# Kernel optimization log

Hardware: AMD Instinct MI355X
Metric: run time of the kernel (lower is better)

The kernel has to match this reference:

```python
import jax, jax.numpy as jnp
import numpy as np

H = 2048
I = 8192
E = 8
EI = I // E  # expert_intermediate_size = 1024


def setup_inputs() -> dict:
    key = jax.random.key(0)
    k1, k2, k3 = jax.random.split(key, 3)
    B, N = 4, 4096
    x = jax.random.normal(k1, (B, N, H), dtype=jnp.float32)
    position_ids = jnp.arange(B * N, dtype=jnp.int64).reshape(B, N)
    gate_up_proj = 0.02 * jax.random.normal(k2, (E, H, EI * 2), dtype=jnp.float32)
    down_proj = 0.02 * jax.random.normal(k3, (E, EI, H), dtype=jnp.float32)
    return {"x": x, "position_ids": position_ids,
            "gate_up_proj": gate_up_proj, "down_proj": down_proj}


def reference(x, position_ids, gate_up_proj, down_proj):
    # x: [B,N,H]; position_ids: [B,N] (or [N]); expert = pos % E.
    B, N, Hdim = x.shape
    if position_ids.ndim == 1:
        position_ids = jnp.broadcast_to(position_ids[None, :], (B, N))
    eids = (position_ids % E).reshape(B * N)
    flat = x.reshape(B * N, Hdim)

    # Modulo routing is perfectly balanced (N % E == 0 with sequential ids),
    # so group tokens by expert (stable sort) and run dense per-expert GEMMs
    # instead of per-token gathered-weight bmm (same math, no weight blowup).
    T = B * N
    order = jnp.argsort(eids)          # stable in jax -> tokens grouped by expert
    xg = flat[order].reshape(E, T // E, Hdim)            # [E, T/E, H]
    gu = jnp.einsum('ebh,ehk->ebk', xg, gate_up_proj)    # [E, T/E, 2*EI]
    gate, up = gu[..., :EI], gu[..., EI:]
    inter = jax.nn.silu(gate) * up                       # [E, T/E, EI]
    outg = jnp.einsum('ebi,eih->ebh', inter, down_proj)  # [E, T/E, H]
    out = jnp.zeros((T, Hdim), dtype=x.dtype).at[order].set(outg.reshape(T, Hdim))
    return out.reshape(B, N, Hdim)
```

## Files before the change

### kernel.cpp

```cpp
#include <hip/hip_runtime.h>
#include <hip/hip_bf16.h>

typedef unsigned short u16;
typedef __attribute__((ext_vector_type(8))) short short8;
typedef __attribute__((ext_vector_type(8))) unsigned short u16x8;
typedef __attribute__((ext_vector_type(4))) float f32x4;

#define H_DIM 2048
#define EI_DIM 1024
#define NEXP 8

template <int V> struct IC { static constexpr int value = V; };

__device__ __forceinline__ u16 f2bf(float f) {
  __hip_bfloat16 h = __float2bfloat16(f);
  return __builtin_bit_cast(unsigned short, h);
}

__device__ __forceinline__ void load_lds16(const void* g, void* lds) {
  __builtin_amdgcn_global_load_lds(
      (const __attribute__((address_space(1))) unsigned int*)g,
      (__attribute__((address_space(3))) unsigned int*)lds, 16, 0, 0);
}

__global__ void hist_kernel(const int* __restrict__ pid, int* __restrict__ hist) {
  int seg = blockIdx.x, lane = threadIdx.x;
  int eid = pid[seg * 64 + lane] & 7;
#pragma unroll
  for (int e = 0; e < NEXP; ++e) {
    unsigned long long m = __ballot(eid == e);
    if (lane == 0) hist[e * 256 + seg] = __popcll(m);
  }
}

__global__ void scan_kernel(const int* __restrict__ hist, int* __restrict__ base,
                            int* __restrict__ offcnt, int T) {
  __shared__ int lds[256];
  int tid = threadIdx.x;
  int v[8], s = 0;
#pragma unroll
  for (int j = 0; j < 8; ++j) { v[j] = hist[tid * 8 + j]; s += v[j]; }
  lds[tid] = s;
  __syncthreads();
  for (int d = 1; d < 256; d <<= 1) {
    int t = (tid >= d) ? lds[tid - d] : 0;
    __syncthreads();
    lds[tid] += t;
    __syncthreads();
  }
  int run = lds[tid] - s;
#pragma unroll
  for (int j = 0; j < 8; ++j) { base[tid * 8 + j] = run; run += v[j]; }
  __syncthreads();
  if (tid < NEXP) {
    int o = base[tid * 256];
    int nx = (tid < NEXP - 1) ? base[(tid + 1) * 256] : T;
    offcnt[tid] = o;
    offcnt[8 + tid] = nx - o;
  }
}

__global__ void rank_kernel(const int* __restrict__ pid, const int* __restrict__ base,
                            int* __restrict__ order) {
  int seg = blockIdx.x, lane = threadIdx.x;
  int t = seg * 64 + lane;
  int eid = pid[t] & 7;
  unsigned long long below = (1ull << lane) - 1ull;
#pragma unroll
  for (int e = 0; e < NEXP; ++e) {
    unsigned long long m = __ballot(eid == e);
    if (eid == e) {
      int r = __popcll(m & below);
      order[base[e * 256 + seg] + r] = t;
    }
  }
}

__global__ __launch_bounds__(256) void transpose_bf16(const float* __restrict__ in,
                                                      u16* __restrict__ out, int R, int C) {
  __shared__ u16 tile[64][65];
  int nbr = R >> 6, nbc = C >> 6;
  int per_e = nbr * nbc;
  int bx = blockIdx.x;
  int e = bx / per_e, rem = bx % per_e;
  int tr = rem % nbr, tc = rem / nbr;
  const float* ine = in + (size_t)e * R * C;
  u16* oute = out + (size_t)e * R * C;
  int r0 = tr * 64, c0 = tc * 64;
  int tid = threadIdx.x;
  int lrow = tid >> 4, lc4 = (tid & 15) * 4;
#pragma unroll
  for (int p = 0; p < 4; ++p) {
    int rl = p * 16 + lrow;
    float4 v = *(const float4*)&ine[(size_t)(r0 + rl) * C + c0 + lc4];
    tile[rl][lc4 + 0] = f2bf(v.x);
    tile[rl][lc4 + 1] = f2bf(v.y);
    tile[rl][lc4 + 2] = f2bf(v.z);
    tile[rl][lc4 + 3] = f2bf(v.w);
  }
  __syncthreads();
#pragma unroll
  for (int q = 0; q < 16; ++q) {
    int idx = q * 256 + tid;
    int jr = idx >> 6, hc = idx & 63;
    oute[(size_t)(c0 + jr) * R + r0 + hc] = tile[hc][jr];
  }
}

__global__ __launch_bounds__(256) void gather_x(const float* __restrict__ x,
                                                const int* __restrict__ order,
                                                u16* __restrict__ xg) {
  int g = blockIdx.x;
  int t = order[g];
  const float* src = x + (size_t)t * H_DIM;
  u16* dst = xg + (size_t)g * H_DIM;
  int c = threadIdx.x * 8;
  float4 a = *(const float4*)&src[c];
  float4 b = *(const float4*)&src[c + 4];
  u16x8 v;
  v[0] = f2bf(a.x); v[1] = f2bf(a.y); v[2] = f2bf(a.z); v[3] = f2bf(a.w);
  v[4] = f2bf(b.x); v[5] = f2bf(b.y); v[6] = f2bf(b.z); v[7] = f2bf(b.w);
  *(u16x8*)&dst[c] = v;
}

template <int KTOT, int KIND>
__device__ __forceinline__ void gemm8_body(
    const u16* __restrict__ A, const u16* __restrict__ Bmat, void* __restrict__ outp,
    const int* __restrict__ offcnt, const int* __restrict__ order, int T) {
  constexpr int NK = KTOT / 64;
  constexpr int ASTR = (KIND == 0) ? H_DIM : EI_DIM;
  constexpr int BSTR = ASTR;
  constexpr size_t BEXP = (size_t)2048 * BSTR;
  __shared__ u16 As[2][2][8192];
  __shared__ u16 Bs[2][2][8192];

  int nwg = gridDim.x;
  int bid = blockIdx.x;
  int bx = (bid & 7) * (nwg >> 3) + (bid >> 3);
  int e = bx >> 6;
  int s = bx & 63;
  int off = offcnt[e], cnt = offcnt[8 + e];
  const u16* Be = Bmat + (size_t)e * BEXP;

  int tid = threadIdx.x, w = tid >> 6, l = tid & 63;
  int wm = w >> 2, wn = w & 3, lr = l & 15, lg = l >> 4;
  int cidx = (lg ^ ((lr >> 1) & 3)) * 8;
  int aRow0 = wm * 128 + lr;
  int bRow0 = wn * 64 + lr;
  int sr[2], sc[2];
#pragma unroll
  for (int j = 0; j < 2; ++j) {
    sr[j] = j * 128 + (tid >> 2);
    int c = tid & 3;
    sc[j] = (c ^ ((sr[j] >> 1) & 3)) * 8;
  }

#pragma unroll 1
  for (int it = s; it < 512; it += 64) {
    int mt = it >> 3, nt = it & 7;
    if (mt * 256 >= cnt) continue;

    const u16* aSrc[2];
    const u16* bSrc[2];
#pragma unroll
    for (int j = 0; j < 2; ++j) {
      int r = sr[j];
      int grow = min(off + mt * 256 + r, T - 1);
      aSrc[j] = A + (size_t)grow * ASTR + sc[j];
      int n;
      if (KIND == 0) {
        int q = r >> 4, rr = r & 15;
        n = ((q & 2) ? EI_DIM : 0) + nt * 128 + ((q >> 2) << 5) + ((q & 1) << 4) + rr;
      } else {
        n = nt * 256 + r;
      }
      bSrc[j] = Be + (size_t)n * BSTR + sc[j];
    }

    auto stageA = [&](int kt, int kh, int buf) {
#pragma unroll
      for (int j = 0; j < 2; ++j)
        load_lds16(aSrc[j] + kt * 64 + kh * 32, &As[buf][kh][j * 4096 + w * 512]);
    };
    auto stageB = [&](int kt, int kh, int buf) {
#pragma unroll
      for (int j = 0; j < 2; ++j)
        load_lds16(bSrc[j] + kt * 64 + kh * 32, &Bs[buf][kh][j * 4096 + w * 512]);
    };

    short8 av[4], bv[4];
    auto loadA4 = [&](int buf, int kh, int h) {
#pragma unroll
      for (int mm = 0; mm < 4; ++mm)
        av[mm] = *(const short8*)&As[buf][kh][(aRow0 + (h * 4 + mm) * 16) * 32 + cidx];
    };
    auto loadB4 = [&](int buf, int kh) {
#pragma unroll
      for (int nn = 0; nn < 4; ++nn)
        bv[nn] = *(const short8*)&Bs[buf][kh][(bRow0 + nn * 16) * 32 + cidx];
    };

    f32x4 acc[8][4];
#pragma unroll
    for (int m = 0; m < 8; ++m)
#pragma unroll
      for (int nn = 0; nn < 4; ++nn) acc[m][nn] = {0.f, 0.f, 0.f, 0.f};

    auto MFMA_H = [&](auto HC) {
      constexpr int h = decltype(HC)::value;
      __builtin_amdgcn_s_setprio(1);
#pragma unroll
      for (int mm = 0; mm < 4; ++mm)
#pragma unroll
        for (int nn = 0; nn < 4; ++nn)
          acc[h * 4 + mm][nn] =
              __builtin_amdgcn_mfma_f32_16x16x32_bf16(av[mm], bv[nn], acc[h * 4 + mm][nn], 0, 0, 0);
      __builtin_amdgcn_s_setprio(0);
    };

    __syncthreads();

    stageA(0, 0, 0); stageB(0, 0, 0); stageA(0, 1, 0); stageB(0, 1, 0);
    stageB(1, 0, 1); stageA(1, 0, 1); stageB(1, 1, 1);
    asm volatile("s_waitcnt vmcnt(6)" ::: "memory");
    __builtin_amdgcn_s_barrier();
    __builtin_amdgcn_sched_barrier(0);

    auto TILE = [&](int t, auto BC) {
      constexpr int b = decltype(BC)::value;
      constexpr int bn = b ^ 1;
      loadA4(b, 0, 0);
      loadB4(b, 0);
      stageA(t + 1, 1, bn);
      __builtin_amdgcn_s_barrier();
      MFMA_H(IC<0>{});
      __builtin_amdgcn_s_barrier();
      loadA4(b, 0, 1);
      stageB(t + 2, 0, b);
      __builtin_amdgcn_s_barrier();
      MFMA_H(IC<1>{});
      __builtin_amdgcn_s_barrier();
      loadA4(b, 1, 0);
      loadB4(b, 1);
      stageA(t + 2, 0, b);
      __builtin_amdgcn_s_barrier();
      MFMA_H(IC<0>{});
      __builtin_amdgcn_s_barrier();
      loadA4(b, 1, 1);
      stageB(t + 2, 1, b);
      __builtin_amdgcn_s_barrier();
      MFMA_H(IC<1>{});
      asm volatile("s_waitcnt vmcnt(6)" ::: "memory");
      __builtin_amdgcn_s_barrier();
    };

#pragma unroll 1
    for (int t = 0; t < NK - 3; t += 2) {
      TILE(t, IC<0>{});
      TILE(t + 1, IC<1>{});
    }

    {
      loadA4(0, 0, 0);
      loadB4(0, 0);
      stageA(NK - 1, 1, 1);
      MFMA_H(IC<0>{});
      loadA4(0, 0, 1);
      MFMA_H(IC<1>{});
      loadA4(0, 1, 0);
      loadB4(0, 1);
      MFMA_H(IC<0>{});
      loadA4(0, 1, 1);
      MFMA_H(IC<1>{});
      asm volatile("s_waitcnt vmcnt(0)" ::: "memory");
      __builtin_amdgcn_s_barrier();
      loadA4(1, 0, 0);
      loadB4(1, 0);
      MFMA_H(IC<0>{});
      loadA4(1, 0, 1);
      MFMA_H(IC<1>{});
      loadA4(1, 1, 0);
      loadB4(1, 1);
      MFMA_H(IC<0>{});
      loadA4(1, 1, 1);
      MFMA_H(IC<1>{});
    }

    if (KIND == 0) {
      u16* inter = (u16*)outp;
#pragma unroll
      for (int m = 0; m < 8; ++m)
#pragma unroll
        for (int nn = 0; nn < 2; ++nn) {
          f32x4 g = acc[m][nn], u = acc[m][nn + 2];
          int icol = nt * 128 + wn * 32 + nn * 16 + lr;
#pragma unroll
          for (int j = 0; j < 4; ++j) {
            int r = wm * 128 + m * 16 + lg * 4 + j;
            int grow = mt * 256 + r;
            if (grow < cnt) {
              float gv = g[j];
              float val = (gv / (1.f + __expf(-gv))) * u[j];
              inter[(size_t)(off + grow) * EI_DIM + icol] = f2bf(val);
            }
          }
        }
    } else {
      float* out = (float*)outp;
      float* lf = (float*)&As[0][0][0];
#pragma unroll
      for (int m = 0; m < 8; ++m) {
        __syncthreads();
#pragma unroll
        for (int nn = 0; nn < 4; ++nn)
#pragma unroll
          for (int j = 0; j < 4; ++j)
            lf[(wm * 16 + lg * 4 + j) * 256 + wn * 64 + nn * 16 + lr] = acc[m][nn][j];
        __syncthreads();
#pragma unroll
        for (int k = 0; k < 4; ++k) {
          int idx = tid + k * 512;
          int rl = idx >> 6, c4 = idx & 63;
          int grow = mt * 256 + (rl >> 4) * 128 + m * 16 + (rl & 15);
          if (grow < cnt) {
            int tt = order[off + grow];
            *(float4*)&out[(size_t)tt * H_DIM + nt * 256 + c4 * 4] =
                *(const float4*)&lf[rl * 256 + c4 * 4];
          }
        }
      }
    }
  }
}

__global__ __launch_bounds__(512, 2) void gemm_gu_kernel(
    const u16* __restrict__ A, const u16* __restrict__ Bmat, void* __restrict__ outp,
    const int* __restrict__ offcnt, int T) {
  gemm8_body<2048, 0>(A, Bmat, outp, offcnt, nullptr, T);
}

__global__ __launch_bounds__(512, 2) void gemm_down_kernel(
    const u16* __restrict__ A, const u16* __restrict__ Bmat, void* __restrict__ outp,
    const int* __restrict__ offcnt, const int* __restrict__ order, int T) {
  gemm8_body<1024, 1>(A, Bmat, outp, offcnt, order, T);
}

extern "C" void kernel_launch(void* const* d_in, const int* in_sizes, int n_in,
                              void* d_out, int out_size, void* d_ws, size_t ws_size,
                              hipStream_t stream) {
  const float* x = (const float*)d_in[0];
  const int* pid = (const int*)d_in[1];
  const float* gup = (const float*)d_in[2];
  const float* dwn = (const float*)d_in[3];
  float* out = (float*)d_out;

  const int T = in_sizes[1];

  char* ws = (char*)d_ws;
  size_t o = 0;
  auto take = [&](size_t b) { size_t r = o; o += (b + 255) & ~(size_t)255; return r; };
  int* offcnt = (int*)(ws + take(32 * 4));
  int* hist = (int*)(ws + take(2048 * 4));
  int* base = (int*)(ws + take(2052 * 4));
  int* order = (int*)(ws + take((size_t)T * 4));
  u16* xg = (u16*)(ws + take((size_t)T * H_DIM * 2));
  u16* wguT = (u16*)(ws + take((size_t)NEXP * 2048 * 2048 * 2));
  u16* wdT = (u16*)(ws + take((size_t)NEXP * 2048 * 1024 * 2));
  u16* inter = (u16*)(ws + take((size_t)T * EI_DIM * 2));

  hist_kernel<<<T / 64, 64, 0, stream>>>(pid, hist);
  scan_kernel<<<1, 256, 0, stream>>>(hist, base, offcnt, T);
  rank_kernel<<<T / 64, 64, 0, stream>>>(pid, base, order);
  transpose_bf16<<<NEXP * 32 * 32, 256, 0, stream>>>(gup, wguT, 2048, 2048);
  transpose_bf16<<<NEXP * 16 * 32, 256, 0, stream>>>(dwn, wdT, 1024, 2048);
  gather_x<<<T, 256, 0, stream>>>(x, order, xg);

  gemm_gu_kernel<<<512, 512, 0, stream>>>(xg, wguT, inter, offcnt, T);
  gemm_down_kernel<<<512, 512, 0, stream>>>(inter, wdT, out, offcnt, order, T);
}
```

Before: 334.8 us.

## Double-buffer MFMA register fragments to overlap LDS reads with matrix ops

Splits the A/B register fragments into two ping-pong sets so the next LDS read can be issued while MFMAs on the current set run. Removes half of the workgroup barriers in the main tile loop and moves the vmcnt wait earlier. This aims to hide LDS read latency and cut barrier stalls. In exchange it raises VGPR pressure and makes the LDS buffer reuse ordering harder to keep race-free.

```diff
diff --git a/kernel.cpp b/kernel.cpp
--- a/kernel.cpp
+++ b/kernel.cpp
@@ -188,16 +188,16 @@
         load_lds16(bSrc[j] + kt * 64 + kh * 32, &Bs[buf][kh][j * 4096 + w * 512]);
     };
 
-    short8 av[4], bv[4];
-    auto loadA4 = [&](int buf, int kh, int h) {
+    short8 avA[4], avB[4], bvA[4], bvB[4];
+    auto RDA = [&](short8(&dst)[4], int buf, int kh, int h) {
 #pragma unroll
       for (int mm = 0; mm < 4; ++mm)
-        av[mm] = *(const short8*)&As[buf][kh][(aRow0 + (h * 4 + mm) * 16) * 32 + cidx];
-    };
-    auto loadB4 = [&](int buf, int kh) {
+        dst[mm] = *(const short8*)&As[buf][kh][(aRow0 + (h * 4 + mm) * 16) * 32 + cidx];
+    };
+    auto RDB = [&](short8(&dst)[4], int buf, int kh) {
 #pragma unroll
       for (int nn = 0; nn < 4; ++nn)
-        bv[nn] = *(const short8*)&Bs[buf][kh][(bRow0 + nn * 16) * 32 + cidx];
+        dst[nn] = *(const short8*)&Bs[buf][kh][(bRow0 + nn * 16) * 32 + cidx];
     };
 
     f32x4 acc[8][4];
@@ -206,7 +206,7 @@
 #pragma unroll
       for (int nn = 0; nn < 4; ++nn) acc[m][nn] = {0.f, 0.f, 0.f, 0.f};
 
-    auto MFMA_H = [&](auto HC) {
+    auto MF = [&](short8(&a)[4], short8(&b)[4], auto HC) {
       constexpr int h = decltype(HC)::value;
       __builtin_amdgcn_s_setprio(1);
 #pragma unroll
@@ -214,7 +214,7 @@
 #pragma unroll
         for (int nn = 0; nn < 4; ++nn)
           acc[h * 4 + mm][nn] =
-              __builtin_amdgcn_mfma_f32_16x16x32_bf16(av[mm], bv[nn], acc[h * 4 + mm][nn], 0, 0, 0);
+              __builtin_amdgcn_mfma_f32_16x16x32_bf16(a[mm], b[nn], acc[h * 4 + mm][nn], 0, 0, 0);
       __builtin_amdgcn_s_setprio(0);
     };
 
@@ -229,28 +229,24 @@
     auto TILE = [&](int t, auto BC) {
       constexpr int b = decltype(BC)::value;
       constexpr int bn = b ^ 1;
-      loadA4(b, 0, 0);
-      loadB4(b, 0);
+      RDA(avA, b, 0, 0);
+      RDB(bvA, b, 0);
       stageA(t + 1, 1, bn);
-      __builtin_amdgcn_s_barrier();
-      MFMA_H(IC<0>{});
-      __builtin_amdgcn_s_barrier();
-      loadA4(b, 0, 1);
+      MF(avA, bvA, IC<0>{});
+      RDA(avB, b, 0, 1);
+      __builtin_amdgcn_s_barrier();
       stageB(t + 2, 0, b);
-      __builtin_amdgcn_s_barrier();
-      MFMA_H(IC<1>{});
-      __builtin_amdgcn_s_barrier();
-      loadA4(b, 1, 0);
-      loadB4(b, 1);
+      MF(avB, bvA, IC<1>{});
+      RDA(avA, b, 1, 0);
+      RDB(bvB, b, 1);
+      __builtin_amdgcn_s_barrier();
       stageA(t + 2, 0, b);
-      __builtin_amdgcn_s_barrier();
-      MFMA_H(IC<0>{});
-      __builtin_amdgcn_s_barrier();
-      loadA4(b, 1, 1);
+      MF(avA, bvB, IC<0>{});
+      asm volatile("s_waitcnt vmcnt(4)" ::: "memory");
+      RDA(avB, b, 1, 1);
+      __builtin_amdgcn_s_barrier();
       stageB(t + 2, 1, b);
-      __builtin_amdgcn_s_barrier();
-      MFMA_H(IC<1>{});
-      asm volatile("s_waitcnt vmcnt(6)" ::: "memory");
+      MF(avB, bvB, IC<1>{});
       __builtin_amdgcn_s_barrier();
     };
 
@@ -261,29 +257,32 @@
     }
 
     {
-      loadA4(0, 0, 0);
-      loadB4(0, 0);
+      RDA(avA, 0, 0, 0);
+      RDB(bvA, 0, 0);
       stageA(NK - 1, 1, 1);
-      MFMA_H(IC<0>{});
-      loadA4(0, 0, 1);
-      MFMA_H(IC<1>{});
-      loadA4(0, 1, 0);
-      loadB4(0, 1);
-      MFMA_H(IC<0>{});
-      loadA4(0, 1, 1);
-      MFMA_H(IC<1>{});
+      MF(avA, bvA, IC<0>{});
+      RDA(avB, 0, 0, 1);
+      __builtin_amdgcn_s_barrier();
+      MF(avB, bvA, IC<1>{});
+      RDA(avA, 0, 1, 0);
+      RDB(bvB, 0, 1);
+      __builtin_amdgcn_s_barrier();
+      MF(avA, bvB, IC<0>{});
       asm volatile("s_waitcnt vmcnt(0)" ::: "memory");
-      __builtin_amdgcn_s_barrier();
-      loadA4(1, 0, 0);
-      loadB4(1, 0);
-      MFMA_H(IC<0>{});
-      loadA4(1, 0, 1);
-      MFMA_H(IC<1>{});
-      loadA4(1, 1, 0);
-      loadB4(1, 1);
-      MFMA_H(IC<0>{});
-      loadA4(1, 1, 1);
-      MFMA_H(IC<1>{});
+      RDA(avB, 0, 1, 1);
+      __builtin_amdgcn_s_barrier();
+      MF(avB, bvB, IC<1>{});
+      __builtin_amdgcn_s_barrier();
+      RDA(avA, 1, 0, 0);
+      RDB(bvA, 1, 0);
+      MF(avA, bvA, IC<0>{});
+      RDA(avB, 1, 0, 1);
+      MF(avB, bvA, IC<1>{});
+      RDA(avA, 1, 1, 0);
+      RDB(bvB, 1, 1);
+      MF(avA, bvB, IC<0>{});
+      RDA(avB, 1, 1, 1);
+      MF(avB, bvB, IC<1>{});
     }
 
     if (KIND == 0) {
```

Result: no change. 333.1 us (median of 2 runs) (-0.5%).
